# Kernel tuning notes

Measured on AMD Instinct MI355X. Metric: run time of the kernel, lower is better.

Reference implementation:

```python
import jax, jax.numpy as jnp
import numpy as np

TWO_PI = 2.0 * np.pi
PI = np.pi
RESONANCE_WEIGHT = 0.1


def setup_inputs() -> dict:
    key = jax.random.key(0)
    k1, k2, k3, k4, k5 = jax.random.split(key, 5)
    B, C = 16384, 1000          # batch, num classes for the CE term
    N, E = 4096, 131072         # graph nodes, directed edges (avg degree 32)
    outputs = jax.random.normal(k1, (B, C), dtype=jnp.float32)
    targets = jax.random.randint(k2, (B,), 0, C)
    resonance_phase = jax.random.normal(k3, (N, N), dtype=jnp.float32)
    edge_src = jax.random.randint(k4, (E,), 0, N)
    edge_dst = jax.random.randint(k5, (E,), 0, N)
    return {"outputs": outputs, "targets": targets,
            "resonance_phase": resonance_phase,
            "edge_src": edge_src, "edge_dst": edge_dst}


def reference(outputs, targets, resonance_phase, edge_src, edge_dst):
    # base_criterion: CrossEntropyLoss (mean reduction over batch)
    logp = jax.nn.log_softmax(outputs, axis=-1)                      # [B, C]
    base_loss = -jnp.mean(jnp.take_along_axis(logp, targets[:, None], axis=1))

    # resonance term: vectorized gather over all topology edges
    phase_ij = resonance_phase[edge_src, edge_dst]                   # [E]
    phase_ji = resonance_phase[edge_dst, edge_src]                   # [E]
    d = jnp.abs(phase_ij - phase_ji) % TWO_PI
    d = jnp.where(d > PI, TWO_PI - d, d)                             # wrap to [0, pi]
    resonance_loss = jnp.sum(d) / d.shape[0]                         # / total_connections

    return base_loss + RESONANCE_WEIGHT * resonance_loss
```

## Files before the change

kernel.cpp:

```cpp
#include <hip/hip_runtime.h>
#include <math.h>

#define TWO_PI_F 6.28318530717958647692f
#define PI_F     3.14159265358979323846f

typedef float f32x4 __attribute__((ext_vector_type(4)));

__device__ __forceinline__ float warp_sum(float s) {
    #pragma unroll
    for (int off = 32; off; off >>= 1) s += __shfl_xor(s, off, 64);
    return s;
}
__device__ __forceinline__ float warp_max(float m) {
    #pragma unroll
    for (int off = 32; off; off >>= 1) m = fmaxf(m, __shfl_xor(m, off, 64));
    return m;
}

__device__ __forceinline__ float max4(f32x4 v) {
    return fmaxf(fmaxf(v.x, v.y), fmaxf(v.z, v.w));
}

__device__ float ce_row_generic(const float* __restrict__ rowp, int C, int lane, int t) {
    const float4* row4 = (const float4*)rowp;
    const int nf4 = C >> 2;
    const float tv = rowp[t];
    float m = -INFINITY;
    for (int j = lane; j < nf4; j += 64) {
        float4 x = row4[j];
        m = fmaxf(m, fmaxf(fmaxf(x.x, x.y), fmaxf(x.z, x.w)));
    }
    const int remBase = nf4 << 2;
    if (remBase + lane < C) m = fmaxf(m, rowp[remBase + lane]);
    m = warp_max(m);
    float s = 0.0f;
    for (int j = lane; j < nf4; j += 64) {
        float4 x = row4[j];
        s += __expf(x.x - m) + __expf(x.y - m) + __expf(x.z - m) + __expf(x.w - m);
    }
    if (remBase + lane < C) s += __expf(rowp[remBase + lane] - m);
    s = warp_sum(s);
    return m + __logf(s) - tv;
}

__global__ __launch_bounds__(256) void fused_kernel(
    const float* __restrict__ outputs,
    const int*   __restrict__ targets,
    const float* __restrict__ phase,
    const int*   __restrict__ esrc,
    const int*   __restrict__ edst,
    int B, int C, int N, int E,
    int res_blocks,
    float invB, float scaleE,
    float* __restrict__ ws)
{
    __shared__ float part[4];
    const int lane = threadIdx.x & 63;
    const int wave = threadIdx.x >> 6;

    float wsum = 0.0f;

    if ((int)blockIdx.x < res_blocks) {
        const int i = blockIdx.x * blockDim.x + threadIdx.x;
        float d = 0.0f;
        if (i < E) {
            const int s = esrc[i];
            const int t = edst[i];
            const float a = phase[(size_t)s * (size_t)N + (size_t)t];
            const float b = phase[(size_t)t * (size_t)N + (size_t)s];
            d = fabsf(a - b);
            d = fmodf(d, TWO_PI_F);
            if (d > PI_F) d = TWO_PI_F - d;
        }
        d = warp_sum(d);
        if (lane == 0) wsum = d * scaleE;
    } else {
        const int row = (blockIdx.x - res_blocks) * 4 + wave;
        if (row < B) {
            const int nf4 = C >> 2;
            const int t = targets[row];
            const float* rowp = outputs + (size_t)row * (size_t)C;
            if (nf4 <= 256) {
                const f32x4* row4 = (const f32x4*)rowp;
                const f32x4 NEG = {-INFINITY, -INFINITY, -INFINITY, -INFINITY};
                const int j0 = lane, j1 = lane + 64, j2 = lane + 128, j3 = lane + 192;
                f32x4 v0 = (j0 < nf4) ? __builtin_nontemporal_load(row4 + j0) : NEG;
                f32x4 v1 = (j1 < nf4) ? __builtin_nontemporal_load(row4 + j1) : NEG;
                f32x4 v2 = (j2 < nf4) ? __builtin_nontemporal_load(row4 + j2) : NEG;
                f32x4 v3 = (j3 < nf4) ? __builtin_nontemporal_load(row4 + j3) : NEG;
                const int remBase = nf4 << 2;
                float tail = (remBase + lane < C)
                           ? __builtin_nontemporal_load(rowp + remBase + lane)
                           : -INFINITY;

                const int fj   = t >> 2;
                const int slot = t & 3;
                int owner;
                float cand;
                if (fj < nf4) {
                    owner = fj & 63;
                    const int reg = fj >> 6;
                    f32x4 c4 = (reg == 0) ? v0 : (reg == 1) ? v1 : (reg == 2) ? v2 : v3;
                    cand = (slot == 0) ? c4.x : (slot == 1) ? c4.y
                         : (slot == 2) ? c4.z : c4.w;
                } else {
                    owner = t - remBase;
                    cand = tail;
                }
                const float tv = __shfl(cand, owner, 64);

                float m = tail;
                m = fmaxf(m, max4(v0));
                m = fmaxf(m, max4(v1));
                m = fmaxf(m, max4(v2));
                m = fmaxf(m, max4(v3));
                m = warp_max(m);

                float s;
                s  = __expf(v0.x - m) + __expf(v0.y - m) + __expf(v0.z - m) + __expf(v0.w - m);
                s += __expf(v1.x - m) + __expf(v1.y - m) + __expf(v1.z - m) + __expf(v1.w - m);
                s += __expf(v2.x - m) + __expf(v2.y - m) + __expf(v2.z - m) + __expf(v2.w - m);
                s += __expf(v3.x - m) + __expf(v3.y - m) + __expf(v3.z - m) + __expf(v3.w - m);
                s += __expf(tail - m);
                s = warp_sum(s);

                if (lane == 0) wsum = (m + __logf(s) - tv) * invB;
            } else {
                const float c = ce_row_generic(rowp, C, lane, t);
                if (lane == 0) wsum = c * invB;
            }
        }
    }

    if (lane == 0) part[wave] = wsum;
    __syncthreads();
    if (threadIdx.x == 0)
        ws[blockIdx.x] = part[0] + part[1] + part[2] + part[3];
}

__global__ __launch_bounds__(256) void reduce_kernel(
    const float* __restrict__ ws, int P, float* __restrict__ out)
{
    float s = 0.0f;
    for (int i = threadIdx.x; i < P; i += 256)
        s += ws[i];
    s = warp_sum(s);
    __shared__ float part[4];
    if ((threadIdx.x & 63) == 0) part[threadIdx.x >> 6] = s;
    __syncthreads();
    if (threadIdx.x == 0)
        out[0] = part[0] + part[1] + part[2] + part[3];
}

extern "C" void kernel_launch(void* const* d_in, const int* in_sizes, int n_in,
                              void* d_out, int out_size, void* d_ws, size_t ws_size,
                              hipStream_t stream) {
    const float* outputs = (const float*)d_in[0];
    const int*   targets = (const int*)d_in[1];
    const float* phase   = (const float*)d_in[2];
    const int*   esrc    = (const int*)d_in[3];
    const int*   edst    = (const int*)d_in[4];

    const int B = in_sizes[1];
    const int C = in_sizes[0] / B;
    const int E = in_sizes[3];
    int N = 1;
    while ((long long)N * (long long)N < (long long)in_sizes[2]) N++;

    const int res_blocks = (E + 255) / 256;
    const int ce_blocks  = (B + 3) / 4;
    const int grid = res_blocks + ce_blocks;

    float* ws = (float*)d_ws;

    fused_kernel<<<grid, 256, 0, stream>>>(outputs, targets, phase, esrc, edst,
                                           B, C, N, E, res_blocks,
                                           1.0f / (float)B, 0.1f / (float)E,
                                           ws);
    reduce_kernel<<<1, 256, 0, stream>>>(ws, grid, (float*)d_out);
}
```

Baseline: 145.5 us.

## Process four CE rows per wave with software-prefetched next row

Each wave now handles four consecutive cross-entropy rows and issues loads for the next row before computing the current one, so memory latency overlaps with the exp/reduction work. This cuts the CE block count by four, which also shrinks the partial-sum array, and the final reduce kernel is widened to 512 threads. In exchange, fewer blocks and higher register pressure may reduce occupancy and parallelism on a memory-bound workload.

After: 143.1 us. No clear change (-1.6%).

```diff
diff --git a/kernel.cpp b/kernel.cpp
--- a/kernel.cpp
+++ b/kernel.cpp
@@ -3,6 +3,7 @@
 
 #define TWO_PI_F 6.28318530717958647692f
 #define PI_F     3.14159265358979323846f
+#define CE_ROWS  4
 
 typedef float f32x4 __attribute__((ext_vector_type(4)));
 
@@ -16,9 +17,44 @@
     for (int off = 32; off; off >>= 1) m = fmaxf(m, __shfl_xor(m, off, 64));
     return m;
 }
-
 __device__ __forceinline__ float max4(f32x4 v) {
     return fmaxf(fmaxf(v.x, v.y), fmaxf(v.z, v.w));
+}
+
+__device__ __forceinline__ float ce_compute(f32x4 v0, f32x4 v1, f32x4 v2, f32x4 v3,
+                                            float tail, int t, int nf4, int remBase,
+                                            int lane) {
+    const int fj   = t >> 2;
+    const int slot = t & 3;
+    int owner;
+    float cand;
+    if (fj < nf4) {
+        owner = fj & 63;
+        const int reg = fj >> 6;
+        f32x4 c4 = (reg == 0) ? v0 : (reg == 1) ? v1 : (reg == 2) ? v2 : v3;
+        cand = (slot == 0) ? c4.x : (slot == 1) ? c4.y : (slot == 2) ? c4.z : c4.w;
+    } else {
+        owner = t - remBase;
+        cand = tail;
+    }
+    const float tv = __shfl(cand, owner, 64);
+
+    float m = tail;
+    m = fmaxf(m, max4(v0));
+    m = fmaxf(m, max4(v1));
+    m = fmaxf(m, max4(v2));
+    m = fmaxf(m, max4(v3));
+    m = warp_max(m);
+
+    float s;
+    s  = __expf(v0.x - m) + __expf(v0.y - m) + __expf(v0.z - m) + __expf(v0.w - m);
+    s += __expf(v1.x - m) + __expf(v1.y - m) + __expf(v1.z - m) + __expf(v1.w - m);
+    s += __expf(v2.x - m) + __expf(v2.y - m) + __expf(v2.z - m) + __expf(v2.w - m);
+    s += __expf(v3.x - m) + __expf(v3.y - m) + __expf(v3.z - m) + __expf(v3.w - m);
+    s += __expf(tail - m);
+    s = warp_sum(s);
+
+    return m + __logf(s) - tv;
 }
 
 __device__ float ce_row_generic(const float* __restrict__ rowp, int C, int lane, int t) {
@@ -75,59 +111,57 @@
         d = warp_sum(d);
         if (lane == 0) wsum = d * scaleE;
     } else {
-        const int row = (blockIdx.x - res_blocks) * 4 + wave;
-        if (row < B) {
-            const int nf4 = C >> 2;
-            const int t = targets[row];
-            const float* rowp = outputs + (size_t)row * (size_t)C;
+        const int nf4 = C >> 2;
+        const int wbase = (((int)blockIdx.x - res_blocks) * 4 + wave) * CE_ROWS;
+        if (wbase < B) {
             if (nf4 <= 256) {
-                const f32x4* row4 = (const f32x4*)rowp;
+                const int remBase = nf4 << 2;
+                const int j0 = lane, j1 = lane + 64, j2 = lane + 128, j3 = lane + 192;
                 const f32x4 NEG = {-INFINITY, -INFINITY, -INFINITY, -INFINITY};
-                const int j0 = lane, j1 = lane + 64, j2 = lane + 128, j3 = lane + 192;
-                f32x4 v0 = (j0 < nf4) ? __builtin_nontemporal_load(row4 + j0) : NEG;
-                f32x4 v1 = (j1 < nf4) ? __builtin_nontemporal_load(row4 + j1) : NEG;
-                f32x4 v2 = (j2 < nf4) ? __builtin_nontemporal_load(row4 + j2) : NEG;
-                f32x4 v3 = (j3 < nf4) ? __builtin_nontemporal_load(row4 + j3) : NEG;
-                const int remBase = nf4 << 2;
-                float tail = (remBase + lane < C)
-                           ? __builtin_nontemporal_load(rowp + remBase + lane)
-                           : -INFINITY;
-
-                const int fj   = t >> 2;
-                const int slot = t & 3;
-                int owner;
-                float cand;
-                if (fj < nf4) {
-                    owner = fj & 63;
-                    const int reg = fj >> 6;
-                    f32x4 c4 = (reg == 0) ? v0 : (reg == 1) ? v1 : (reg == 2) ? v2 : v3;
-                    cand = (slot == 0) ? c4.x : (slot == 1) ? c4.y
-                         : (slot == 2) ? c4.z : c4.w;
-                } else {
-                    owner = t - remBase;
-                    cand = tail;
+
+                const float* rp = outputs + (size_t)wbase * (size_t)C;
+                const f32x4* r4 = (const f32x4*)rp;
+                f32x4 a0 = (j0 < nf4) ? __builtin_nontemporal_load(r4 + j0) : NEG;
+                f32x4 a1 = (j1 < nf4) ? __builtin_nontemporal_load(r4 + j1) : NEG;
+                f32x4 a2 = (j2 < nf4) ? __builtin_nontemporal_load(r4 + j2) : NEG;
+                f32x4 a3 = (j3 < nf4) ? __builtin_nontemporal_load(r4 + j3) : NEG;
+                float atail = (remBase + lane < C)
+                            ? __builtin_nontemporal_load(rp + remBase + lane)
+                            : -INFINITY;
+                int   at = targets[wbase];
+
+                float acc = 0.0f;
+                #pragma unroll
+                for (int k = 0; k < CE_ROWS; ++k) {
+                    const int row = wbase + k;
+                    f32x4 b0 = NEG, b1 = NEG, b2 = NEG, b3 = NEG;
+                    float btail = -INFINITY;
+                    int   bt = 0;
+                    if (k + 1 < CE_ROWS && row + 1 < B) {
+                        const float* np = outputs + (size_t)(row + 1) * (size_t)C;
+                        const f32x4* n4 = (const f32x4*)np;
+                        bt = targets[row + 1];
+                        if (j0 < nf4) b0 = __builtin_nontemporal_load(n4 + j0);
+                        if (j1 < nf4) b1 = __builtin_nontemporal_load(n4 + j1);
+                        if (j2 < nf4) b2 = __builtin_nontemporal_load(n4 + j2);
+                        if (j3 < nf4) b3 = __builtin_nontemporal_load(n4 + j3);
+                        if (remBase + lane < C)
+                            btail = __builtin_nontemporal_load(np + remBase + lane);
+                    }
+                    if (row < B)
+                        acc += ce_compute(a0, a1, a2, a3, atail, at, nf4, remBase, lane);
+                    a0 = b0; a1 = b1; a2 = b2; a3 = b3; atail = btail; at = bt;
                 }
-                const float tv = __shfl(cand, owner, 64);
-
-                float m = tail;
-                m = fmaxf(m, max4(v0));
-                m = fmaxf(m, max4(v1));
-                m = fmaxf(m, max4(v2));
-                m = fmaxf(m, max4(v3));
-                m = warp_max(m);
-
-                float s;
-                s  = __expf(v0.x - m) + __expf(v0.y - m) + __expf(v0.z - m) + __expf(v0.w - m);
-                s += __expf(v1.x - m) + __expf(v1.y - m) + __expf(v1.z - m) + __expf(v1.w - m);
-                s += __expf(v2.x - m) + __expf(v2.y - m) + __expf(v2.z - m) + __expf(v2.w - m);
-                s += __expf(v3.x - m) + __expf(v3.y - m) + __expf(v3.z - m) + __expf(v3.w - m);
-                s += __expf(tail - m);
-                s = warp_sum(s);
-
-                if (lane == 0) wsum = (m + __logf(s) - tv) * invB;
+                if (lane == 0) wsum = acc * invB;
             } else {
-                const float c = ce_row_generic(rowp, C, lane, t);
-                if (lane == 0) wsum = c * invB;
+                float acc = 0.0f;
+                for (int k = 0; k < CE_ROWS; ++k) {
+                    const int row = wbase + k;
+                    if (row < B)
+                        acc += ce_row_generic(outputs + (size_t)row * (size_t)C,
+                                              C, lane, targets[row]);
+                }
+                if (lane == 0) wsum = acc * invB;
             }
         }
     }
@@ -138,18 +172,22 @@
         ws[blockIdx.x] = part[0] + part[1] + part[2] + part[3];
 }
 
-__global__ __launch_bounds__(256) void reduce_kernel(
+__global__ __launch_bounds__(512) void reduce_kernel(
     const float* __restrict__ ws, int P, float* __restrict__ out)
 {
     float s = 0.0f;
-    for (int i = threadIdx.x; i < P; i += 256)
+    for (int i = threadIdx.x; i < P; i += 512)
         s += ws[i];
     s = warp_sum(s);
-    __shared__ float part[4];
+    __shared__ float part[8];
     if ((threadIdx.x & 63) == 0) part[threadIdx.x >> 6] = s;
     __syncthreads();
-    if (threadIdx.x == 0)
-        out[0] = part[0] + part[1] + part[2] + part[3];
+    if (threadIdx.x == 0) {
+        float tot = 0.0f;
+        #pragma unroll
+        for (int i = 0; i < 8; i++) tot += part[i];
+        out[0] = tot;
+    }
 }
 
 extern "C" void kernel_launch(void* const* d_in, const int* in_sizes, int n_in,
@@ -168,7 +206,8 @@
     while ((long long)N * (long long)N < (long long)in_sizes[2]) N++;
 
     const int res_blocks = (E + 255) / 256;
-    const int ce_blocks  = (B + 3) / 4;
+    const int rows_per_block = 4 * CE_ROWS;
+    const int ce_blocks  = (B + rows_per_block - 1) / rows_per_block;
     const int grid = res_blocks + ce_blocks;
 
     float* ws = (float*)d_ws;
@@ -177,5 +216,5 @@
                                            B, C, N, E, res_blocks,
                                            1.0f / (float)B, 0.1f / (float)E,
                                            ws);
-    reduce_kernel<<<1, 256, 0, stream>>>(ws, grid, (float*)d_out);
-}
+    reduce_kernel<<<1, 512, 0, stream>>>(ws, grid, (float*)d_out);
+}
```
